# Kernel tuning notes

Measured on AMD Instinct MI355X. Metric: run time of the kernel, lower is better.

Reference implementation:

```python
import jax, jax.numpy as jnp
import numpy as np

SQRT2 = 1.4142135623730951  # lrelu def_gain
LRELU_SLOPE = 0.2
EPS = 1e-8


def setup_inputs() -> dict:
    key = jax.random.key(0)
    k1, k2, k3, k4 = jax.random.split(key, 4)
    B, C_in, C_out, H, W, K, DLAT = 8, 512, 512, 32, 32, 3, 512
    x = jax.random.normal(k1, (B, C_in, H, W), dtype=jnp.float32)
    y = jax.random.normal(k2, (B, DLAT), dtype=jnp.float32)
    # init_std = 1.0 since use_wscale=True, lrmul=1
    weight = jax.random.normal(k3, (C_out, C_in, K, K), dtype=jnp.float32)
    mod_weight = jax.random.normal(k4, (C_in, DLAT), dtype=jnp.float32)
    bias = jnp.ones((C_in,), dtype=jnp.float32)
    return {"x": x, "y": y, "weight": weight, "mod_weight": mod_weight, "bias": bias}


def reference(x, y, weight, mod_weight, bias):
    B, C_in, H, W = x.shape
    C_out, _, K, _ = weight.shape
    dlat = mod_weight.shape[1]
    w_mul_mod = dlat ** (-0.5)  # EqualizedLinear wscale; conv w_mul is unused in forward
    # style: s = sqrt(2) * lrelu(y @ W_mod^T + b)
    s = y @ (mod_weight * w_mul_mod).T  # [B, C_in]
    s = jax.nn.leaky_relu(s + bias, LRELU_SLOPE) * SQRT2
    # modulate per-sample weights: [B, C_out, C_in, K, K]
    ww = weight[None] * s[:, None, :, None, None]
    # demodulate
    d = jax.lax.rsqrt(jnp.sum(ww * ww, axis=(2, 3, 4)) + EPS)  # [B, C_out]
    ww = ww * d[:, :, None, None, None]
    # fused grouped conv: groups = batch
    xg = x.reshape(1, B * C_in, H, W)
    wg = ww.reshape(B * C_out, C_in, K, K)
    out = jax.lax.conv_general_dilated(
        xg, wg, window_strides=(1, 1), padding="SAME",
        dimension_numbers=("NCHW", "OIHW", "NCHW"),
        feature_group_count=B)
    return out.reshape(B, C_out, H, W)
```

## Files before the change

### kernel.cpp

```cpp
#include <hip/hip_runtime.h>
#include <hip/hip_bf16.h>

typedef float f32x4 __attribute__((ext_vector_type(4)));
typedef short bf16x8 __attribute__((ext_vector_type(8)));

#define LRELU_SLOPE 0.2f
#define SQRT2F 1.4142135623730951f
#define MODSCALE 0.044194173824159216f

#define GLL(SRC, DST)                                                       \
  __builtin_amdgcn_global_load_lds(                                         \
      (const __attribute__((address_space(1))) unsigned int*)(SRC),         \
      (__attribute__((address_space(3))) unsigned int*)(DST), 16, 0, 0)

__global__ __launch_bounds__(256) void prep_kernel(const float* __restrict__ w,
                                                   const float* __restrict__ y,
                                                   const float* __restrict__ mw,
                                                   const float* __restrict__ bias,
                                                   __hip_bfloat16* __restrict__ wt,
                                                   float* __restrict__ wsq,
                                                   float* __restrict__ s,
                                                   __hip_bfloat16* __restrict__ xsp) {
  const int bid = blockIdx.x;
  const int tid = threadIdx.x;
  if (bid < 1024) {
    int idx = bid * 256 + tid;
    const float* p = w + (size_t)idx * 9;
    float v[9];
    float sq = 0.f;
#pragma unroll
    for (int t = 0; t < 9; ++t) {
      v[t] = p[t];
      sq += v[t] * v[t];
    }
    wsq[idx] = sq;
#pragma unroll
    for (int t = 0; t < 9; ++t) wt[t * 262144 + idx] = __float2bfloat16(v[t]);
  } else if (bid < 1152) {
    int l = tid & 63;
    int ci = (bid - 1024) * 4 + (tid >> 6);
    const float4* mwr = reinterpret_cast<const float4*>(mw + ci * 512);
    float4 m0 = mwr[2 * l], m1 = mwr[2 * l + 1];
    float acc[8];
#pragma unroll
    for (int b = 0; b < 8; ++b) {
      const float4* yr = reinterpret_cast<const float4*>(y + b * 512);
      float4 y0 = yr[2 * l], y1 = yr[2 * l + 1];
      acc[b] = m0.x * y0.x + m0.y * y0.y + m0.z * y0.z + m0.w * y0.w +
               m1.x * y1.x + m1.y * y1.y + m1.z * y1.z + m1.w * y1.w;
    }
#pragma unroll
    for (int off = 32; off > 0; off >>= 1) {
#pragma unroll
      for (int b = 0; b < 8; ++b) acc[b] += __shfl_xor(acc[b], off, 64);
    }
    if (l < 8) {
      float v = acc[l] * MODSCALE + bias[ci];
      v = v > 0.f ? v : LRELU_SLOPE * v;
      s[l * 512 + ci] = v * SQRT2F;
    }
  } else {
    int i = (bid - 1152) * 256 + tid;
    int b = i / 8448;
    int r = i - b * 8448;
    int pos = r >> 6;
    int cj = (r & 63) << 3;
    int hr, hc;
    if (pos < 34) { hr = 0; hc = pos; }
    else if (pos < 68) { hr = 33; hc = pos - 34; }
    else if (pos < 100) { hr = pos - 67; hc = 0; }
    else { hr = pos - 99; hc = 33; }
    unsigned off = (unsigned)((b * 34 + hr) * 34 + hc) * 512 + cj;
    int4 z = {0, 0, 0, 0};
    *reinterpret_cast<int4*>(xsp + off) = z;
  }
}

__global__ __launch_bounds__(256) void xsdem_kernel(const float* __restrict__ x,
                                                    const float* __restrict__ s,
                                                    const float* __restrict__ wsq,
                                                    __hip_bfloat16* __restrict__ xsp,
                                                    float* __restrict__ d) {
  const int bid = blockIdx.x;
  const int tid = threadIdx.x;
  if (bid < 2048) {
    int cc = bid & 7;
    int h = (bid >> 3) & 31;
    int b = bid >> 8;
    __shared__ __hip_bfloat16 tile[32][72];
    int cil = tid >> 2;
    int w0 = (tid & 3) * 8;
    int ci = cc * 64 + cil;
    const float* xp = x + (((size_t)(b * 512 + ci) * 32 + h) << 5) + w0;
    float sv = s[b * 512 + ci];
    float4 a0 = *reinterpret_cast<const float4*>(xp);
    float4 a1 = *reinterpret_cast<const float4*>(xp + 4);
    tile[w0 + 0][cil] = __float2bfloat16(a0.x * sv);
    tile[w0 + 1][cil] = __float2bfloat16(a0.y * sv);
    tile[w0 + 2][cil] = __float2bfloat16(a0.z * sv);
    tile[w0 + 3][cil] = __float2bfloat16(a0.w * sv);
    tile[w0 + 4][cil] = __float2bfloat16(a1.x * sv);
    tile[w0 + 5][cil] = __float2bfloat16(a1.y * sv);
    tile[w0 + 6][cil] = __float2bfloat16(a1.z * sv);
    tile[w0 + 7][cil] = __float2bfloat16(a1.w * sv);
    __syncthreads();
    int wloc = tid >> 3;
    int cj = (tid & 7) * 8;
    int4 v = *reinterpret_cast<const int4*>(&tile[wloc][cj]);
    unsigned off = (unsigned)((b * 34 + h + 1) * 34 + (wloc + 1)) * 512 + cc * 64 + cj;
    *reinterpret_cast<int4*>(xsp + off) = v;
  } else {
    int l = tid & 63;
    int co = (bid - 2048) * 4 + (tid >> 6);
    const float4* qr = reinterpret_cast<const float4*>(wsq + co * 512);
    float4 q0 = qr[2 * l], q1 = qr[2 * l + 1];
    float acc[8];
#pragma unroll
    for (int b = 0; b < 8; ++b) {
      const float4* sr = reinterpret_cast<const float4*>(s + b * 512);
      float4 s0 = sr[2 * l], s1 = sr[2 * l + 1];
      acc[b] = q0.x * s0.x * s0.x + q0.y * s0.y * s0.y + q0.z * s0.z * s0.z +
               q0.w * s0.w * s0.w + q1.x * s1.x * s1.x + q1.y * s1.y * s1.y +
               q1.z * s1.z * s1.z + q1.w * s1.w * s1.w;
    }
#pragma unroll
    for (int off = 32; off > 0; off >>= 1) {
#pragma unroll
      for (int b = 0; b < 8; ++b) acc[b] += __shfl_xor(acc[b], off, 64);
    }
    if (l < 8) d[l * 512 + co] = rsqrtf(acc[l] + 1e-8f);
  }
}

__global__ __launch_bounds__(512, 2) void conv_kernel(const __hip_bfloat16* __restrict__ xsp,
                                                      const __hip_bfloat16* __restrict__ wt,
                                                      const float* __restrict__ dmod,
                                                      float* __restrict__ out) {
  __shared__ __hip_bfloat16 As_[2][224 * 64];
  __shared__ __hip_bfloat16 Bs_[4][128 * 64];
  const int bid = blockIdx.x;
  const int xcd = bid & 7, slot0 = bid >> 3;
  const int bm = xcd * 8 + (slot0 >> 2);
  const int bn = slot0 & 3;
  const int tid = threadIdx.x;
  const int wv = tid >> 6;
  const int l = tid & 63;
  const int kg = wv >> 2;
  const int wr = (wv >> 1) & 1, wc = wv & 1;
  const int bb = bm >> 3;
  const int h0 = (bm & 7) << 2;

  const int swz = (((l & 7) ^ (l >> 3)) << 3);
  unsigned boff[2];
#pragma unroll
  for (int j = 0; j < 2; ++j) {
    int row = ((j * 8 + wv) << 3) + (l >> 3);
    boff[j] = (unsigned)((bn << 7) + row) * 512 + swz;
  }
  unsigned ahoff[4];
  int adst[4];
#pragma unroll
  for (int j = 0; j < 4; ++j) {
    int rb = j < 3 ? j * 64 + wv * 8 : 192 + (wv & 3) * 8;
    int r = rb + (l >> 3);
    int rc = r > 203 ? 203 : r;
    int hr = rc / 34, hc = rc - hr * 34;
    ahoff[j] = (unsigned)((bb * 34 + h0 + hr) * 34 + hc) * 512 + (((l & 7) ^ (r & 7)) << 3);
    adst[j] = rb;
  }
  int pb[4];
#pragma unroll
  for (int m = 0; m < 4; ++m)
    pb[m] = ((wr << 1) + (m >> 1)) * 34 + ((m & 1) << 4) + (l & 15);

  f32x4 acc[4][4];
#pragma unroll
  for (int n = 0; n < 4; ++n)
#pragma unroll
    for (int m = 0; m < 4; ++m) acc[n][m] = (f32x4)0.f;

  auto stageB = [&](int sl, int t, int k0c) {
    const __hip_bfloat16* src = wt + t * 262144 + k0c * 64;
#pragma unroll
    for (int j = 0; j < 2; ++j)
      GLL(src + boff[j], &Bs_[sl][(j * 8 + wv) << 9]);
  };
  auto stageA1 = [&](int ab, int j, int kn) {
    GLL(xsp + ahoff[j] + kn * 64, &As_[ab][adst[j] << 6]);
  };
  auto phase = [&](int ab, int sl, int dh, int dw) {
    const int cb = (kg << 2) + (l >> 4);
    bf16x8 af[4], bfr[4];
#pragma unroll
    for (int m = 0; m < 4; ++m) {
      int p = pb[m] + dh * 34 + dw;
      af[m] = *reinterpret_cast<const bf16x8*>(&As_[ab][p * 64 + ((cb ^ (p & 7)) << 3)]);
    }
#pragma unroll
    for (int n = 0; n < 4; ++n) {
      int row = (wc << 6) + (n << 4) + (l & 15);
      bfr[n] = *reinterpret_cast<const bf16x8*>(&Bs_[sl][row * 64 + ((cb ^ (l & 7)) << 3)]);
    }
    __builtin_amdgcn_s_setprio(1);
#pragma unroll
    for (int n = 0; n < 4; ++n)
#pragma unroll
      for (int m = 0; m < 4; ++m)
        acc[n][m] = __builtin_amdgcn_mfma_f32_16x16x32_bf16(bfr[n], af[m], acc[n][m], 0, 0, 0);
    __builtin_amdgcn_s_setprio(0);
  };

#define SB0 __builtin_amdgcn_sched_barrier(0)
#define WB(N)                                               \
  asm volatile("s_waitcnt vmcnt(" #N ")" ::: "memory");     \
  __builtin_amdgcn_s_barrier();                             \
  SB0

#pragma unroll
  for (int j = 0; j < 4; ++j) stageA1(0, j, 0);
  SB0;
  stageB(0, 0, 0);
  stageB(1, 1, 0);
  stageB(2, 2, 0);

#pragma unroll 1
  for (int k0 = 0; k0 < 7; ++k0) {
    const int a = k0 & 1, an = a ^ 1, kn = k0 + 1;
    WB(4); stageB((k0 + 3) & 3, 3, k0); stageA1(an, 0, kn); SB0; phase(a, (k0 + 0) & 3, 0, 0);
    WB(5); stageB((k0 + 4) & 3, 4, k0); stageA1(an, 1, kn); SB0; phase(a, (k0 + 1) & 3, 0, 1);
    WB(6); stageB((k0 + 5) & 3, 5, k0); stageA1(an, 2, kn); SB0; phase(a, (k0 + 2) & 3, 0, 2);
    WB(7); stageB((k0 + 6) & 3, 6, k0); stageA1(an, 3, kn); SB0; phase(a, (k0 + 3) & 3, 1, 0);
    WB(7); stageB((k0 + 7) & 3, 7, k0); SB0; phase(a, (k0 + 4) & 3, 1, 1);
    WB(6); stageB((k0 + 8) & 3, 8, k0); SB0; phase(a, (k0 + 5) & 3, 1, 2);
    WB(5); stageB((k0 + 9) & 3, 0, kn); SB0; phase(a, (k0 + 6) & 3, 2, 0);
    WB(4); stageB((k0 + 10) & 3, 1, kn); SB0; phase(a, (k0 + 7) & 3, 2, 1);
    WB(4); stageB((k0 + 11) & 3, 2, kn); SB0; phase(a, (k0 + 8) & 3, 2, 2);
  }
  {
    WB(4); stageB((7 + 3) & 3, 3, 7); SB0; phase(1, (7 + 0) & 3, 0, 0);
    WB(4); stageB((7 + 4) & 3, 4, 7); SB0; phase(1, (7 + 1) & 3, 0, 1);
    WB(4); stageB((7 + 5) & 3, 5, 7); SB0; phase(1, (7 + 2) & 3, 0, 2);
    WB(4); stageB((7 + 6) & 3, 6, 7); SB0; phase(1, (7 + 3) & 3, 1, 0);
    WB(4); stageB((7 + 7) & 3, 7, 7); SB0; phase(1, (7 + 4) & 3, 1, 1);
    WB(4); stageB((7 + 8) & 3, 8, 7); SB0; phase(1, (7 + 5) & 3, 1, 2);
    WB(4); SB0; phase(1, (7 + 6) & 3, 2, 0);
    WB(2); SB0; phase(1, (7 + 7) & 3, 2, 1);
    WB(0); SB0; phase(1, (7 + 8) & 3, 2, 2);
  }
#undef WB
#undef SB0

  float* red = reinterpret_cast<float*>(&Bs_[0][0]);
  __syncthreads();
  if (kg == 1) {
#pragma unroll
    for (int n = 0; n < 4; ++n)
#pragma unroll
      for (int m = 0; m < 4; ++m)
        *reinterpret_cast<f32x4*>(red + (n * 4 + m) * 1024 + (wv & 3) * 256 + l * 4) =
            acc[n][m];
  }
  __syncthreads();
  if (kg == 0) {
    const int pixbase = ((bm & 7) << 7) + (wr << 6) + (l & 15);
    const int cob = (bn << 7) + (wc << 6) + ((l >> 4) << 2);
    float* ob = out + ((size_t)bb << 19);
    const float* drow = dmod + bb * 512;
#pragma unroll
    for (int n = 0; n < 4; ++n) {
#pragma unroll
      for (int m = 0; m < 4; ++m)
        acc[n][m] += *reinterpret_cast<const f32x4*>(red + (n * 4 + m) * 1024 + wv * 256 + l * 4);
#pragma unroll
      for (int jj = 0; jj < 4; ++jj) {
        const int co = cob + (n << 4) + jj;
        const float dv = drow[co];
        float* orow = ob + ((unsigned)co << 10) + pixbase;
#pragma unroll
        for (int m = 0; m < 4; ++m) orow[m << 4] = acc[n][m][jj] * dv;
      }
    }
  }
}

extern "C" void kernel_launch(void* const* d_in, const int* in_sizes, int n_in,
                              void* d_out, int out_size, void* d_ws, size_t ws_size,
                              hipStream_t stream) {
  (void)in_sizes; (void)n_in; (void)out_size; (void)ws_size;
  const float* x = (const float*)d_in[0];
  const float* y = (const float*)d_in[1];
  const float* w = (const float*)d_in[2];
  const float* mw = (const float*)d_in[3];
  const float* bias = (const float*)d_in[4];
  float* out = (float*)d_out;

  char* ws = (char*)d_ws;
  float* s = (float*)(ws + 0);
  float* dmod = (float*)(ws + 16384);
  float* wsq = (float*)(ws + 32768);
  __hip_bfloat16* wt = (__hip_bfloat16*)(ws + 1081344);
  __hip_bfloat16* xsp = (__hip_bfloat16*)(ws + 5799936);

  prep_kernel<<<1416, 256, 0, stream>>>(w, y, mw, bias, wt, wsq, s, xsp);
  xsdem_kernel<<<2176, 256, 0, stream>>>(x, s, wsq, xsp, dmod);
  conv_kernel<<<256, 512, 0, stream>>>(xsp, wt, dmod, out);
}
```

Measured before the change: 71.38 us.

## Double-buffer MFMA fragments to overlap LDS reads with matrix math

Restructures the implicit-GEMM conv main loop so the LDS fragment reads for the next tap go into a second register bank, issued before the MFMAs of the current tap run. The loop is unrolled by two K-chunks (18 taps) so the bank indices and waitcnt values are compile-time constants. The vmcnt/barrier schedule is reworked to match. The goal is to hide LDS read latency behind MFMA execution, at the cost of extra VGPRs, a larger unrolled body, and more delicate synchronisation.

```diff
diff --git a/kernel.cpp b/kernel.cpp
--- a/kernel.cpp
+++ b/kernel.cpp
@@ -179,6 +179,8 @@
 #pragma unroll
     for (int m = 0; m < 4; ++m) acc[n][m] = (f32x4)0.f;
 
+  bf16x8 fa[2][4], fb[2][4];
+
   auto stageB = [&](int sl, int t, int k0c) {
     const __hip_bfloat16* src = wt + t * 262144 + k0c * 64;
 #pragma unroll
@@ -188,67 +190,79 @@
   auto stageA1 = [&](int ab, int j, int kn) {
     GLL(xsp + ahoff[j] + kn * 64, &As_[ab][adst[j] << 6]);
   };
-  auto phase = [&](int ab, int sl, int dh, int dw) {
+  auto readfrag = [&](int bk, int ab, int sl, int dh, int dw) {
     const int cb = (kg << 2) + (l >> 4);
-    bf16x8 af[4], bfr[4];
 #pragma unroll
     for (int m = 0; m < 4; ++m) {
       int p = pb[m] + dh * 34 + dw;
-      af[m] = *reinterpret_cast<const bf16x8*>(&As_[ab][p * 64 + ((cb ^ (p & 7)) << 3)]);
+      fa[bk][m] = *reinterpret_cast<const bf16x8*>(&As_[ab][p * 64 + ((cb ^ (p & 7)) << 3)]);
     }
 #pragma unroll
     for (int n = 0; n < 4; ++n) {
       int row = (wc << 6) + (n << 4) + (l & 15);
-      bfr[n] = *reinterpret_cast<const bf16x8*>(&Bs_[sl][row * 64 + ((cb ^ (l & 7)) << 3)]);
-    }
+      fb[bk][n] = *reinterpret_cast<const bf16x8*>(&Bs_[sl][row * 64 + ((cb ^ (l & 7)) << 3)]);
+    }
+  };
+  auto mfmacl = [&](int bk) {
     __builtin_amdgcn_s_setprio(1);
 #pragma unroll
     for (int n = 0; n < 4; ++n)
 #pragma unroll
       for (int m = 0; m < 4; ++m)
-        acc[n][m] = __builtin_amdgcn_mfma_f32_16x16x32_bf16(bfr[n], af[m], acc[n][m], 0, 0, 0);
+        acc[n][m] = __builtin_amdgcn_mfma_f32_16x16x32_bf16(fb[bk][n], fa[bk][m], acc[n][m], 0, 0, 0);
     __builtin_amdgcn_s_setprio(0);
   };
-
-#define SB0 __builtin_amdgcn_sched_barrier(0)
-#define WB(N)                                               \
-  asm volatile("s_waitcnt vmcnt(" #N ")" ::: "memory");     \
-  __builtin_amdgcn_s_barrier();                             \
-  SB0
+  auto waitbar = [&](int n) {
+    if (n == 0) asm volatile("s_waitcnt vmcnt(0)" ::: "memory");
+    else if (n == 2) asm volatile("s_waitcnt vmcnt(2)" ::: "memory");
+    else if (n == 3) asm volatile("s_waitcnt vmcnt(3)" ::: "memory");
+    else asm volatile("s_waitcnt vmcnt(4)" ::: "memory");
+    __builtin_amdgcn_s_barrier();
+    __builtin_amdgcn_sched_barrier(0);
+  };
+  auto body = [&](int uC, int cbase, bool stA) {
+    const int t = uC % 9;
+    const int bank = uC & 1;
+    const int N = ((uC + 8) % 9 < 4) ? 3 : 2;
+    waitbar(N);
+    const int t3 = (uC + 3) % 9;
+    stageB((cbase + uC + 3) & 3, t3, cbase + (uC + 3) / 9);
+    if (stA && t < 4) stageA1(((uC / 9) & 1) ^ 1, t, cbase + uC / 9 + 1);
+    __builtin_amdgcn_sched_barrier(0);
+    const int t1 = (uC + 1) % 9;
+    readfrag(bank ^ 1, ((uC + 1) / 9) & 1, (cbase + uC + 1) & 3, t1 / 3, t1 % 3);
+    __builtin_amdgcn_sched_barrier(0);
+    mfmacl(bank);
+  };
+  auto body7 = [&](int uC) {
+    const int bank = (uC + 1) & 1;
+    waitbar(uC >= 7 ? 0 : 2);
+    if (uC < 6) stageB((uC + 2) & 3, uC + 3, 7);
+    __builtin_amdgcn_sched_barrier(0);
+    if (uC < 8) readfrag(bank ^ 1, 1, uC & 3, (uC + 1) / 3, (uC + 1) % 3);
+    __builtin_amdgcn_sched_barrier(0);
+    mfmacl(bank);
+  };
 
 #pragma unroll
   for (int j = 0; j < 4; ++j) stageA1(0, j, 0);
-  SB0;
+  __builtin_amdgcn_sched_barrier(0);
   stageB(0, 0, 0);
   stageB(1, 1, 0);
   stageB(2, 2, 0);
+  waitbar(4);
+  readfrag(0, 0, 0, 0, 0);
+  __builtin_amdgcn_sched_barrier(0);
 
 #pragma unroll 1
-  for (int k0 = 0; k0 < 7; ++k0) {
-    const int a = k0 & 1, an = a ^ 1, kn = k0 + 1;
-    WB(4); stageB((k0 + 3) & 3, 3, k0); stageA1(an, 0, kn); SB0; phase(a, (k0 + 0) & 3, 0, 0);
-    WB(5); stageB((k0 + 4) & 3, 4, k0); stageA1(an, 1, kn); SB0; phase(a, (k0 + 1) & 3, 0, 1);
-    WB(6); stageB((k0 + 5) & 3, 5, k0); stageA1(an, 2, kn); SB0; phase(a, (k0 + 2) & 3, 0, 2);
-    WB(7); stageB((k0 + 6) & 3, 6, k0); stageA1(an, 3, kn); SB0; phase(a, (k0 + 3) & 3, 1, 0);
-    WB(7); stageB((k0 + 7) & 3, 7, k0); SB0; phase(a, (k0 + 4) & 3, 1, 1);
-    WB(6); stageB((k0 + 8) & 3, 8, k0); SB0; phase(a, (k0 + 5) & 3, 1, 2);
-    WB(5); stageB((k0 + 9) & 3, 0, kn); SB0; phase(a, (k0 + 6) & 3, 2, 0);
-    WB(4); stageB((k0 + 10) & 3, 1, kn); SB0; phase(a, (k0 + 7) & 3, 2, 1);
-    WB(4); stageB((k0 + 11) & 3, 2, kn); SB0; phase(a, (k0 + 8) & 3, 2, 2);
-  }
-  {
-    WB(4); stageB((7 + 3) & 3, 3, 7); SB0; phase(1, (7 + 0) & 3, 0, 0);
-    WB(4); stageB((7 + 4) & 3, 4, 7); SB0; phase(1, (7 + 1) & 3, 0, 1);
-    WB(4); stageB((7 + 5) & 3, 5, 7); SB0; phase(1, (7 + 2) & 3, 0, 2);
-    WB(4); stageB((7 + 6) & 3, 6, 7); SB0; phase(1, (7 + 3) & 3, 1, 0);
-    WB(4); stageB((7 + 7) & 3, 7, 7); SB0; phase(1, (7 + 4) & 3, 1, 1);
-    WB(4); stageB((7 + 8) & 3, 8, 7); SB0; phase(1, (7 + 5) & 3, 1, 2);
-    WB(4); SB0; phase(1, (7 + 6) & 3, 2, 0);
-    WB(2); SB0; phase(1, (7 + 7) & 3, 2, 1);
-    WB(0); SB0; phase(1, (7 + 8) & 3, 2, 2);
-  }
-#undef WB
-#undef SB0
+  for (int kp = 0; kp < 3; ++kp) {
+#pragma unroll
+    for (int u = 0; u < 18; ++u) body(u, 2 * kp, true);
+  }
+#pragma unroll
+  for (int u = 0; u < 9; ++u) body(u, 6, true);
+#pragma unroll
+  for (int u = 0; u < 9; ++u) body7(u);
 
   float* red = reinterpret_cast<float*>(&Bs_[0][0]);
   __syncthreads();
```

Measured after the change: 64.33 us. 9.9% less time.

## Restructure conv pipeline to stage three taps per barrier with register double-buffering

Applied to the files above, without the earlier changes.

Replaces the per-tap four-slot weight ring with two LDS buffers that each hold the three kw taps of one kernel row. This cuts the barriers per K-chunk from nine to three. Inside each row, LDS fragment reads are double-buffered in registers so the next tap's reads overlap the current MFMAs. Each wave starts at a different tap (wv%3) to spread LDS bank pressure. The cost is vmcnt(0) full waits at every barrier instead of partial waits, and higher register pressure from the doubled fragment sets.

```diff
diff --git a/kernel.cpp b/kernel.cpp
--- a/kernel.cpp
+++ b/kernel.cpp
@@ -137,7 +137,7 @@
                                                       const float* __restrict__ dmod,
                                                       float* __restrict__ out) {
   __shared__ __hip_bfloat16 As_[2][224 * 64];
-  __shared__ __hip_bfloat16 Bs_[4][128 * 64];
+  __shared__ __hip_bfloat16 Bs_[2][3 * 128 * 64];
   const int bid = blockIdx.x;
   const int xcd = bid & 7, slot0 = bid >> 3;
   const int bm = xcd * 8 + (slot0 >> 2);
@@ -149,6 +149,9 @@
   const int wr = (wv >> 1) & 1, wc = wv & 1;
   const int bb = bm >> 3;
   const int h0 = (bm & 7) << 2;
+  const int start = wv % 3;
+  const int p1r = start == 2 ? 0 : start + 1;
+  const int p2r = 3 - start - p1r;
 
   const int swz = (((l & 7) ^ (l >> 3)) << 3);
   unsigned boff[2];
@@ -179,75 +182,89 @@
 #pragma unroll
     for (int m = 0; m < 4; ++m) acc[n][m] = (f32x4)0.f;
 
-  auto stageB = [&](int sl, int t, int k0c) {
+  bf16x8 fa[2][4], fb[2][4];
+
+  auto stageB = [&](__hip_bfloat16* Bn, int t, int k0c) {
     const __hip_bfloat16* src = wt + t * 262144 + k0c * 64;
 #pragma unroll
     for (int j = 0; j < 2; ++j)
-      GLL(src + boff[j], &Bs_[sl][(j * 8 + wv) << 9]);
+      GLL(src + boff[j], Bn + ((j * 8 + wv) << 9));
   };
-  auto stageA1 = [&](int ab, int j, int kn) {
-    GLL(xsp + ahoff[j] + kn * 64, &As_[ab][adst[j] << 6]);
+  auto stageA1 = [&](__hip_bfloat16* An, int j, int kn) {
+    GLL(xsp + ahoff[j] + kn * 64, An + (adst[j] << 6));
   };
-  auto phase = [&](int ab, int sl, int dh, int dw) {
+  auto readfrag = [&](int bk, const __hip_bfloat16* Aq, const __hip_bfloat16* Bq,
+                      int dh, int dw) {
     const int cb = (kg << 2) + (l >> 4);
-    bf16x8 af[4], bfr[4];
 #pragma unroll
     for (int m = 0; m < 4; ++m) {
       int p = pb[m] + dh * 34 + dw;
-      af[m] = *reinterpret_cast<const bf16x8*>(&As_[ab][p * 64 + ((cb ^ (p & 7)) << 3)]);
+      fa[bk][m] = *reinterpret_cast<const bf16x8*>(Aq + p * 64 + ((cb ^ (p & 7)) << 3));
     }
 #pragma unroll
     for (int n = 0; n < 4; ++n) {
       int row = (wc << 6) + (n << 4) + (l & 15);
-      bfr[n] = *reinterpret_cast<const bf16x8*>(&Bs_[sl][row * 64 + ((cb ^ (l & 7)) << 3)]);
-    }
+      fb[bk][n] = *reinterpret_cast<const bf16x8*>(Bq + row * 64 + ((cb ^ (l & 7)) << 3));
+    }
+  };
+  auto mfmacl = [&](int bk) {
     __builtin_amdgcn_s_setprio(1);
 #pragma unroll
     for (int n = 0; n < 4; ++n)
 #pragma unroll
       for (int m = 0; m < 4; ++m)
-        acc[n][m] = __builtin_amdgcn_mfma_f32_16x16x32_bf16(bfr[n], af[m], acc[n][m], 0, 0, 0);
+        acc[n][m] = __builtin_amdgcn_mfma_f32_16x16x32_bf16(fb[bk][n], fa[bk][m], acc[n][m], 0, 0, 0);
     __builtin_amdgcn_s_setprio(0);
   };
 
 #define SB0 __builtin_amdgcn_sched_barrier(0)
-#define WB(N)                                               \
-  asm volatile("s_waitcnt vmcnt(" #N ")" ::: "memory");     \
+#define WAITBAR0                                            \
+  asm volatile("s_waitcnt vmcnt(0)" ::: "memory");          \
   __builtin_amdgcn_s_barrier();                             \
   SB0
 
 #pragma unroll
-  for (int j = 0; j < 4; ++j) stageA1(0, j, 0);
+  for (int j = 0; j < 4; ++j) stageA1(&As_[0][0], j, 0);
   SB0;
-  stageB(0, 0, 0);
-  stageB(1, 1, 0);
-  stageB(2, 2, 0);
+  stageB(&Bs_[0][0] + 0 * 8192, 0, 0);
+  stageB(&Bs_[0][0] + 1 * 8192, 1, 0);
+  stageB(&Bs_[0][0] + 2 * 8192, 2, 0);
 
 #pragma unroll 1
-  for (int k0 = 0; k0 < 7; ++k0) {
-    const int a = k0 & 1, an = a ^ 1, kn = k0 + 1;
-    WB(4); stageB((k0 + 3) & 3, 3, k0); stageA1(an, 0, kn); SB0; phase(a, (k0 + 0) & 3, 0, 0);
-    WB(5); stageB((k0 + 4) & 3, 4, k0); stageA1(an, 1, kn); SB0; phase(a, (k0 + 1) & 3, 0, 1);
-    WB(6); stageB((k0 + 5) & 3, 5, k0); stageA1(an, 2, kn); SB0; phase(a, (k0 + 2) & 3, 0, 2);
-    WB(7); stageB((k0 + 6) & 3, 6, k0); stageA1(an, 3, kn); SB0; phase(a, (k0 + 3) & 3, 1, 0);
-    WB(7); stageB((k0 + 7) & 3, 7, k0); SB0; phase(a, (k0 + 4) & 3, 1, 1);
-    WB(6); stageB((k0 + 8) & 3, 8, k0); SB0; phase(a, (k0 + 5) & 3, 1, 2);
-    WB(5); stageB((k0 + 9) & 3, 0, kn); SB0; phase(a, (k0 + 6) & 3, 2, 0);
-    WB(4); stageB((k0 + 10) & 3, 1, kn); SB0; phase(a, (k0 + 7) & 3, 2, 1);
-    WB(4); stageB((k0 + 11) & 3, 2, kn); SB0; phase(a, (k0 + 8) & 3, 2, 2);
-  }
-  {
-    WB(4); stageB((7 + 3) & 3, 3, 7); SB0; phase(1, (7 + 0) & 3, 0, 0);
-    WB(4); stageB((7 + 4) & 3, 4, 7); SB0; phase(1, (7 + 1) & 3, 0, 1);
-    WB(4); stageB((7 + 5) & 3, 5, 7); SB0; phase(1, (7 + 2) & 3, 0, 2);
-    WB(4); stageB((7 + 6) & 3, 6, 7); SB0; phase(1, (7 + 3) & 3, 1, 0);
-    WB(4); stageB((7 + 7) & 3, 7, 7); SB0; phase(1, (7 + 4) & 3, 1, 1);
-    WB(4); stageB((7 + 8) & 3, 8, 7); SB0; phase(1, (7 + 5) & 3, 1, 2);
-    WB(4); SB0; phase(1, (7 + 6) & 3, 2, 0);
-    WB(2); SB0; phase(1, (7 + 7) & 3, 2, 1);
-    WB(0); SB0; phase(1, (7 + 8) & 3, 2, 2);
-  }
-#undef WB
+  for (int k0 = 0; k0 < 8; ++k0) {
+    const __hip_bfloat16* Aq = &As_[k0 & 1][0];
+    __hip_bfloat16* An = &As_[(k0 + 1) & 1][0];
+#pragma unroll
+    for (int dh = 0; dh < 3; ++dh) {
+      __hip_bfloat16* Br = &Bs_[(k0 + dh) & 1][0];
+      __hip_bfloat16* Bo = &Bs_[((k0 + dh) & 1) ^ 1][0];
+      WAITBAR0;
+      if (!(k0 == 7 && dh == 2)) {
+        const int tb = dh < 2 ? (dh + 1) * 3 : 0;
+        const int kc = dh < 2 ? k0 : k0 + 1;
+        stageB(Bo + 0 * 8192, tb + 0, kc);
+        stageB(Bo + 1 * 8192, tb + 1, kc);
+        stageB(Bo + 2 * 8192, tb + 2, kc);
+      }
+      if (k0 < 7) {
+        if (dh == 0) { stageA1(An, 0, k0 + 1); stageA1(An, 1, k0 + 1); }
+        else if (dh == 1) { stageA1(An, 2, k0 + 1); stageA1(An, 3, k0 + 1); }
+      }
+      SB0;
+      readfrag(0, Aq, Br + start * 8192, dh, start);
+      SB0;
+      readfrag(1, Aq, Br + p1r * 8192, dh, p1r);
+      SB0;
+      mfmacl(0);
+      SB0;
+      readfrag(0, Aq, Br + p2r * 8192, dh, p2r);
+      SB0;
+      mfmacl(1);
+      SB0;
+      mfmacl(0);
+    }
+  }
+#undef WAITBAR0
 #undef SB0
 
   float* red = reinterpret_cast<float*>(&Bs_[0][0]);
```

New measurement: 61.35 us. 1.16x faster.

## Load conv weight fragments directly from global into registers, bypassing LDS

Applied to the files above, without the earlier changes.

The weight tensor is re-laid out in the prep kernel into per-tap, per-channel-chunk slabs so that each wave can read its MFMA B fragments straight from global memory into registers. This removes the B staging buffers in LDS and the nine barrier-synchronised stages per chunk. Register double-banking of B fragments is meant to hide the load latency, with a single barrier per K chunk for the A tile. The trade-off is more global/L2 traffic, since weights are no longer shared through LDS across waves, and MFMA stalls if the latency is not covered.

```diff
diff --git a/kernel.cpp b/kernel.cpp
--- a/kernel.cpp
+++ b/kernel.cpp
@@ -17,7 +17,7 @@
                                                    const float* __restrict__ y,
                                                    const float* __restrict__ mw,
                                                    const float* __restrict__ bias,
-                                                   __hip_bfloat16* __restrict__ wt,
+                                                   __hip_bfloat16* __restrict__ wt2,
                                                    float* __restrict__ wsq,
                                                    float* __restrict__ s,
                                                    __hip_bfloat16* __restrict__ xsp) {
@@ -25,6 +25,7 @@
   const int tid = threadIdx.x;
   if (bid < 1024) {
     int idx = bid * 256 + tid;
+    int co = idx >> 9, ci = idx & 511;
     const float* p = w + (size_t)idx * 9;
     float v[9];
     float sq = 0.f;
@@ -34,8 +35,10 @@
       sq += v[t] * v[t];
     }
     wsq[idx] = sq;
-#pragma unroll
-    for (int t = 0; t < 9; ++t) wt[t * 262144 + idx] = __float2bfloat16(v[t]);
+    int slabbase = ((ci >> 6) * 2 + ((ci >> 5) & 1)) * 16384 + co * 32 + (ci & 31);
+#pragma unroll
+    for (int t = 0; t < 9; ++t)
+      wt2[t * 262144 + slabbase] = __float2bfloat16(v[t]);
   } else if (bid < 1152) {
     int l = tid & 63;
     int ci = (bid - 1024) * 4 + (tid >> 6);
@@ -133,11 +136,11 @@
 }
 
 __global__ __launch_bounds__(512, 2) void conv_kernel(const __hip_bfloat16* __restrict__ xsp,
-                                                      const __hip_bfloat16* __restrict__ wt,
+                                                      const __hip_bfloat16* __restrict__ wt2,
                                                       const float* __restrict__ dmod,
                                                       float* __restrict__ out) {
   __shared__ __hip_bfloat16 As_[2][224 * 64];
-  __shared__ __hip_bfloat16 Bs_[4][128 * 64];
+  __shared__ float red[16384];
   const int bid = blockIdx.x;
   const int xcd = bid & 7, slot0 = bid >> 3;
   const int bm = xcd * 8 + (slot0 >> 2);
@@ -150,13 +153,6 @@
   const int bb = bm >> 3;
   const int h0 = (bm & 7) << 2;
 
-  const int swz = (((l & 7) ^ (l >> 3)) << 3);
-  unsigned boff[2];
-#pragma unroll
-  for (int j = 0; j < 2; ++j) {
-    int row = ((j * 8 + wv) << 3) + (l >> 3);
-    boff[j] = (unsigned)((bn << 7) + row) * 512 + swz;
-  }
   unsigned ahoff[4];
   int adst[4];
 #pragma unroll
@@ -173,84 +169,78 @@
   for (int m = 0; m < 4; ++m)
     pb[m] = ((wr << 1) + (m >> 1)) * 34 + ((m & 1) << 4) + (l & 15);
 
+  const char* wtb = reinterpret_cast<const char*>(wt2);
+  const unsigned nbase = (unsigned)(bn << 13) + (wc << 12) + ((l & 15) << 6) + ((l >> 4) << 4);
+
   f32x4 acc[4][4];
 #pragma unroll
   for (int n = 0; n < 4; ++n)
 #pragma unroll
     for (int m = 0; m < 4; ++m) acc[n][m] = (f32x4)0.f;
 
-  auto stageB = [&](int sl, int t, int k0c) {
-    const __hip_bfloat16* src = wt + t * 262144 + k0c * 64;
-#pragma unroll
-    for (int j = 0; j < 2; ++j)
-      GLL(src + boff[j], &Bs_[sl][(j * 8 + wv) << 9]);
-  };
-  auto stageA1 = [&](int ab, int j, int kn) {
-    GLL(xsp + ahoff[j] + kn * 64, &As_[ab][adst[j] << 6]);
-  };
-  auto phase = [&](int ab, int sl, int dh, int dw) {
+  bf16x8 fbk[2][4];
+
+  auto stageA1 = [&](__hip_bfloat16* An, int j, int kn) {
+    GLL(xsp + ahoff[j] + kn * 64, An + (adst[j] << 6));
+  };
+  auto loadB = [&](int bank, int t, int c) {
+    const char* base = wtb + (size_t)(((t * 8 + c) * 2 + kg) << 15) + nbase;
+#pragma unroll
+    for (int n = 0; n < 4; ++n)
+      fbk[bank][n] = *reinterpret_cast<const bf16x8*>(base + (n << 10));
+  };
+  auto doTap = [&](int bank, const __hip_bfloat16* Aq, int dh, int dw) {
     const int cb = (kg << 2) + (l >> 4);
-    bf16x8 af[4], bfr[4];
+    bf16x8 af[4];
 #pragma unroll
     for (int m = 0; m < 4; ++m) {
       int p = pb[m] + dh * 34 + dw;
-      af[m] = *reinterpret_cast<const bf16x8*>(&As_[ab][p * 64 + ((cb ^ (p & 7)) << 3)]);
-    }
-#pragma unroll
-    for (int n = 0; n < 4; ++n) {
-      int row = (wc << 6) + (n << 4) + (l & 15);
-      bfr[n] = *reinterpret_cast<const bf16x8*>(&Bs_[sl][row * 64 + ((cb ^ (l & 7)) << 3)]);
+      af[m] = *reinterpret_cast<const bf16x8*>(Aq + p * 64 + ((cb ^ (p & 7)) << 3));
     }
     __builtin_amdgcn_s_setprio(1);
 #pragma unroll
     for (int n = 0; n < 4; ++n)
 #pragma unroll
       for (int m = 0; m < 4; ++m)
-        acc[n][m] = __builtin_amdgcn_mfma_f32_16x16x32_bf16(bfr[n], af[m], acc[n][m], 0, 0, 0);
+        acc[n][m] = __builtin_amdgcn_mfma_f32_16x16x32_bf16(fbk[bank][n], af[m], acc[n][m], 0, 0, 0);
     __builtin_amdgcn_s_setprio(0);
   };
-
-#define SB0 __builtin_amdgcn_sched_barrier(0)
-#define WB(N)                                               \
-  asm volatile("s_waitcnt vmcnt(" #N ")" ::: "memory");     \
-  __builtin_amdgcn_s_barrier();                             \
-  SB0
-
-#pragma unroll
-  for (int j = 0; j < 4; ++j) stageA1(0, j, 0);
-  SB0;
-  stageB(0, 0, 0);
-  stageB(1, 1, 0);
-  stageB(2, 2, 0);
+  auto chunkBody = [&](int c, int P, bool stA, bool last) {
+    const __hip_bfloat16* Aq = &As_[P][0];
+    __hip_bfloat16* An = &As_[P ^ 1][0];
+#pragma unroll
+    for (int t = 0; t < 9; ++t) {
+      if (!last || t < 8) loadB((P + t + 1) & 1, (t + 1) % 9, t < 8 ? c : c + 1);
+      if (stA && t == 0) {
+        stageA1(An, 0, c + 1); stageA1(An, 1, c + 1);
+        stageA1(An, 2, c + 1); stageA1(An, 3, c + 1);
+        __builtin_amdgcn_sched_barrier(0);
+      }
+      doTap((P + t) & 1, Aq, t / 3, t % 3);
+    }
+    if (!last) {
+      asm volatile("s_waitcnt vmcnt(4)" ::: "memory");
+      __builtin_amdgcn_s_barrier();
+      __builtin_amdgcn_sched_barrier(0);
+    }
+  };
+
+#pragma unroll
+  for (int j = 0; j < 4; ++j) stageA1(&As_[0][0], j, 0);
+  __builtin_amdgcn_sched_barrier(0);
+  loadB(0, 0, 0);
+  asm volatile("s_waitcnt vmcnt(4)" ::: "memory");
+  __builtin_amdgcn_s_barrier();
+  __builtin_amdgcn_sched_barrier(0);
 
 #pragma unroll 1
-  for (int k0 = 0; k0 < 7; ++k0) {
-    const int a = k0 & 1, an = a ^ 1, kn = k0 + 1;
-    WB(4); stageB((k0 + 3) & 3, 3, k0); stageA1(an, 0, kn); SB0; phase(a, (k0 + 0) & 3, 0, 0);
-    WB(5); stageB((k0 + 4) & 3, 4, k0); stageA1(an, 1, kn); SB0; phase(a, (k0 + 1) & 3, 0, 1);
-    WB(6); stageB((k0 + 5) & 3, 5, k0); stageA1(an, 2, kn); SB0; phase(a, (k0 + 2) & 3, 0, 2);
-    WB(7); stageB((k0 + 6) & 3, 6, k0); stageA1(an, 3, kn); SB0; phase(a, (k0 + 3) & 3, 1, 0);
-    WB(7); stageB((k0 + 7) & 3, 7, k0); SB0; phase(a, (k0 + 4) & 3, 1, 1);
-    WB(6); stageB((k0 + 8) & 3, 8, k0); SB0; phase(a, (k0 + 5) & 3, 1, 2);
-    WB(5); stageB((k0 + 9) & 3, 0, kn); SB0; phase(a, (k0 + 6) & 3, 2, 0);
-    WB(4); stageB((k0 + 10) & 3, 1, kn); SB0; phase(a, (k0 + 7) & 3, 2, 1);
-    WB(4); stageB((k0 + 11) & 3, 2, kn); SB0; phase(a, (k0 + 8) & 3, 2, 2);
-  }
-  {
-    WB(4); stageB((7 + 3) & 3, 3, 7); SB0; phase(1, (7 + 0) & 3, 0, 0);
-    WB(4); stageB((7 + 4) & 3, 4, 7); SB0; phase(1, (7 + 1) & 3, 0, 1);
-    WB(4); stageB((7 + 5) & 3, 5, 7); SB0; phase(1, (7 + 2) & 3, 0, 2);
-    WB(4); stageB((7 + 6) & 3, 6, 7); SB0; phase(1, (7 + 3) & 3, 1, 0);
-    WB(4); stageB((7 + 7) & 3, 7, 7); SB0; phase(1, (7 + 4) & 3, 1, 1);
-    WB(4); stageB((7 + 8) & 3, 8, 7); SB0; phase(1, (7 + 5) & 3, 1, 2);
-    WB(4); SB0; phase(1, (7 + 6) & 3, 2, 0);
-    WB(2); SB0; phase(1, (7 + 7) & 3, 2, 1);
-    WB(0); SB0; phase(1, (7 + 8) & 3, 2, 2);
-  }
-#undef WB
-#undef SB0
-
-  float* red = reinterpret_cast<float*>(&Bs_[0][0]);
+  for (int kp = 0; kp < 3; ++kp) {
+    chunkBody(2 * kp, 0, true, false);
+    chunkBody(2 * kp + 1, 1, true, false);
+  }
+  chunkBody(6, 0, true, false);
+  chunkBody(7, 1, false, true);
+
   __syncthreads();
   if (kg == 1) {
 #pragma unroll
@@ -298,10 +288,10 @@
   float* s = (float*)(ws + 0);
   float* dmod = (float*)(ws + 16384);
   float* wsq = (float*)(ws + 32768);
-  __hip_bfloat16* wt = (__hip_bfloat16*)(ws + 1081344);
+  __hip_bfloat16* wt2 = (__hip_bfloat16*)(ws + 1081344);
   __hip_bfloat16* xsp = (__hip_bfloat16*)(ws + 5799936);
 
-  prep_kernel<<<1416, 256, 0, stream>>>(w, y, mw, bias, wt, wsq, s, xsp);
+  prep_kernel<<<1416, 256, 0, stream>>>(w, y, mw, bias, wt2, wsq, s, xsp);
   xsdem_kernel<<<2176, 256, 0, stream>>>(x, s, wsq, xsp, dmod);
-  conv_kernel<<<256, 512, 0, stream>>>(xsp, wt, dmod, out);
-}
+  conv_kernel<<<256, 512, 0, stream>>>(xsp, wt2, dmod, out);
+}
```

After: 59.87 us. 1.19x faster.
